# Optimization experiments

Measured on AMD Instinct MI355X. Metric: run time of the kernel, lower is better.

## Reference

```python
import jax, jax.numpy as jnp
import numpy as np

DN = ('NCHW', 'OIHW', 'NCHW')

def conv(x, w, b, stride=1, pad=0):
    y = jax.lax.conv_general_dilated(x, w, (stride, stride), ((pad, pad), (pad, pad)), dimension_numbers=DN)
    return y + b[None, :, None, None]

def maxpool(x, k, s):
    return jax.lax.reduce_window(x, -jnp.inf, jax.lax.max, (1, 1, k, k), (1, 1, s, s), 'VALID')

def bilinear_resize(x, oh, ow):
    # torch F.interpolate(mode='bilinear', align_corners=False)
    H, W = x.shape[2], x.shape[3]
    def grid(n_in, n_out):
        c = (jnp.arange(n_out, dtype=x.dtype) + 0.5) * (n_in / n_out) - 0.5
        c = jnp.clip(c, 0.0, n_in - 1)
        lo = jnp.floor(c).astype(jnp.int32)
        hi = jnp.minimum(lo + 1, n_in - 1)
        return lo, hi, c - lo
    r0, r1, wr = grid(H, oh)
    c0, c1, wc = grid(W, ow)
    top = x[:, :, r0, :] * (1 - wr)[None, None, :, None] + x[:, :, r1, :] * wr[None, None, :, None]
    return top[:, :, :, c0] * (1 - wc) + top[:, :, :, c1] * wc

def setup_inputs():
    key = jax.random.key(0)
    ks = jax.random.split(key, 18)
    s = 0.02
    d = {}
    d['x'] = jax.random.normal(ks[0], (16, 3, 448, 448), jnp.float32)
    d['w1'] = jax.random.normal(ks[1], (64, 3, 7, 7), jnp.float32) * s
    d['b1'] = jax.random.normal(ks[2], (64,), jnp.float32) * s
    d['w3'] = jax.random.normal(ks[3], (192, 64, 3, 3), jnp.float32) * s
    d['b3'] = jax.random.normal(ks[4], (192,), jnp.float32) * s
    d['w4'] = jax.random.normal(ks[5], (256, 192, 3, 3), jnp.float32) * s
    d['b4'] = jax.random.normal(ks[6], (256,), jnp.float32) * s
    d['w7'] = jax.random.normal(ks[7], (512, 256, 2, 2), jnp.float32) * s
    d['b7'] = jax.random.normal(ks[8], (512,), jnp.float32) * s
    d['w8'] = jax.random.normal(ks[9], (1024, 512, 2, 2), jnp.float32) * s
    d['b8'] = jax.random.normal(ks[10], (1024,), jnp.float32) * s
    d['wu'] = jax.random.normal(ks[11], (1024, 1024, 2, 2), jnp.float32) * s
    d['bu'] = jax.random.normal(ks[12], (1024,), jnp.float32) * s
    d['lc_w'] = jax.random.normal(ks[13], (1024, 256, 7, 7, 3, 3), jnp.float32) * s
    d['lc_b'] = jax.random.normal(ks[14], (256, 7, 7), jnp.float32) * s
    d['fc_w'] = jax.random.normal(ks[15], (4949, 12544), jnp.float32) * s  # S*S*(C+B*5)=7*7*101
    d['fc_b'] = jax.random.normal(ks[16], (4949,), jnp.float32) * s
    return d

def reference(x, w1, b1, w3, b3, w4, b4, w7, b7, w8, b8, wu, bu, lc_w, lc_b, fc_w, fc_b):
    x = conv(x, w1, b1, 2, 3)        # [B,64,224,224]
    x = maxpool(x, 2, 2)             # 112
    x = conv(x, w3, b3, 1, 1)        # [B,192,112,112]
    x = maxpool(x, 2, 2)             # 56
    x = conv(x, w4, b4)              # [B,256,54,54]
    x = maxpool(x, 2, 2)             # 27
    # CombinedNet backbone not defined in source listing: identity (256->256)
    x = conv(x, w7, b7)              # [B,512,26,26]
    x = maxpool(x, 2, 2)             # 13
    x = conv(x, w8, b8)              # [B,1024,12,12]
    x = conv(x, wu, bu)              # 11 (ultblock applied twice, shared weights)
    x = conv(x, wu, bu)              # 10
    x = maxpool(x, 5, 4)             # [B,1024,2,2]
    x = x[:, :, :14, :14]
    x = bilinear_resize(x, 7, 7)     # [B,1024,7,7]
    # LocallyConnected2d(1024,256,7,7,k=3,s=1,p=1) without materializing the unfold*weight product
    B = x.shape[0]
    xp = jnp.pad(x, ((0, 0), (0, 0), (1, 1), (1, 1)))
    patches = jnp.stack([xp[:, :, i:i + 7, j:j + 7] for i in range(3) for j in range(3)], axis=2)
    patches = patches.reshape(B, 1024, 3, 3, 7, 7)  # [B,C,kh,kw,H,W]
    y = jnp.einsum('bcijhw,cohwij->bohw', patches, lc_w) + lc_b[None]
    y = jnp.where(y > 0, y, 0.1 * y)  # LeakyReLU(0.1)
    # Dropout(p=0.5) is identity at inference; Linear
    y = y.reshape(B, -1) @ fc_w.T + fc_b  # [B,4949]
    return y.reshape(B, 7, 7, 101)
```

## Files before the change

### kernel.cpp

```cpp
#include <hip/hip_runtime.h>

#define UNR _Pragma("unroll")

typedef __attribute__((ext_vector_type(8))) short short8v;
typedef __attribute__((ext_vector_type(4))) float f32x4;

__device__ __forceinline__ ushort f2bf(float f) {
    union { float f; unsigned u; } x; x.f = f;
    unsigned r = (x.u + 0x7fffu + ((x.u >> 16) & 1u)) >> 16;
    return (ushort)r;
}
__device__ __forceinline__ float bf2f(ushort u) {
    union { unsigned u; float f; } x; x.u = ((unsigned)u) << 16;
    return x.f;
}

__device__ __forceinline__ void gll16(const ushort* gp, ushort* lp) {
    __builtin_amdgcn_global_load_lds(
        (const __attribute__((address_space(1))) unsigned int*)(const void*)gp,
        (__attribute__((address_space(3))) unsigned int*)(void*)lp, 16, 0, 0);
}

template<int Wp,int Hp,int OW,int OH,int WpN,int HpN,int PADN,int CN,int WAVES>
__global__ __launch_bounds__(WAVES*64)
void convc1(const ushort* __restrict__ Xp, const ushort* __restrict__ Wb,
            const float* __restrict__ bias, ushort* __restrict__ Yp)
{
    constexpr int CIN = 4, STRIDE = 2, NSTEP = 7;
    constexpr int POW = OW/2, POH = OH/2;
    constexpr int NTOT = 16*POW*POH*4;

    const int lane = (int)threadIdx.x & 63;
    const int wave = (int)threadIdx.x >> 6;
    const int n0   = (blockIdx.y*WAVES + wave) * 64;
    const int lm   = lane & 15;
    const int lk   = lane >> 4;

    int ns[4];
    unsigned boff[4];
    UNR for (int nf=0; nf<4; ++nf) {
        int n = n0 + nf*16 + lm;
        if (n > NTOT-1) n = NTOT-1;
        ns[nf] = n;
        int q = n & 3, pp = n >> 2;
        int px = pp % POW; int t = pp / POW;
        int py = t % POH;  int b = t / POH;
        int oy = 2*py + (q>>1), ox = 2*px + (q&1);
        boff[nf] = ((unsigned)(b*Hp + oy*STRIDE)*Wp + (unsigned)(ox*STRIDE))*CIN
                 + 8u*lk;
    }

    f32x4 acc[4][4];
    UNR for (int i=0;i<4;++i) UNR for (int j=0;j<4;++j) acc[i][j] = f32x4{0.f,0.f,0.f,0.f};

    auto ldfr = [&](int s, short8v (&a)[4], short8v (&bf)[4]) {
        const unsigned xoff = (unsigned)(s*Wp*CIN);
        UNR for (int mf=0; mf<4; ++mf)
            a[mf] = *(const short8v*)(Wb + (unsigned)((s*4 + mf)<<9) + (unsigned)lane*8);
        UNR for (int nf=0; nf<4; ++nf)
            bf[nf] = *(const short8v*)(Xp + boff[nf] + xoff);
    };
    auto dm = [&](short8v (&a)[4], short8v (&bf)[4]) {
        UNR for (int mf=0; mf<4; ++mf)
            UNR for (int nf=0; nf<4; ++nf)
                acc[mf][nf] = __builtin_amdgcn_mfma_f32_16x16x32_bf16(
                                  a[mf], bf[nf], acc[mf][nf], 0, 0, 0);
    };

    short8v aA[4], bA[4], aB[4], bB[4];
    ldfr(0, aA, bA);
    for (int sb = 0; sb < NSTEP; sb += 2) {
        if (sb+1 < NSTEP) ldfr(sb+1, aB, bB);
        dm(aA, bA);
        if (sb+2 < NSTEP) ldfr(sb+2, aA, bA);
        if (sb+1 < NSTEP) dm(aB, bB);
    }

    UNR for (int mf=0; mf<4; ++mf) {
        const int co = mf*16 + 4*lk;
        f32x4 bi = *(const f32x4*)(bias + co);
        UNR for (int nf=0; nf<4; ++nf) {
            f32x4 v = acc[mf][nf];
            UNR for (int r=0;r<4;++r) {
                float t2 = v[r] + bi[r];
                t2 = fmaxf(t2, __shfl_xor(t2 = t2, 1, 64));
                t2 = fmaxf(t2, __shfl_xor(t2, 2, 64));
                v[r] = t2;
            }
            if ((lane & 3) == 0 && (n0 + nf*16 + lm) < NTOT) {
                int pp = ns[nf] >> 2;
                int px = pp % POW; int t2 = pp / POW;
                int py = t2 % POH; int b = t2 / POH;
                unsigned off = ((unsigned)(b*HpN + py + PADN)*WpN
                                + (unsigned)(px + PADN))*CN + co;
                ushort4 s; s.x=f2bf(v[0]); s.y=f2bf(v[1]); s.z=f2bf(v[2]); s.w=f2bf(v[3]);
                *(ushort4*)(Yp + off) = s;
            }
        }
    }
}

template<int CIN,int K,int STRIDE,int Wp,int Hp,int OW,int OH,int COUT,
         bool POOL,int WpN,int HpN,int PADN,int CN,int MT,int NT,int SPLITS>
__global__ __launch_bounds__(256)
void convt(const ushort* __restrict__ Xp, const ushort* __restrict__ Wb,
           const float* __restrict__ bias, ushort* __restrict__ Yp,
           float* __restrict__ part)
{
    static_assert(MT*NT == 4, "4 waves");
    constexpr int POW = OW/2, POH = OH/2;
    constexpr int NTOT = POOL ? 16*POW*POH*4 : 16*OW*OH;
    constexpr int NCH = CIN/32, NSTEP = K*K*NCH;
    constexpr int SPS = NSTEP/SPLITS;
    constexpr int CA = MT*4, CPW = MT + NT;

    const int t    = (int)threadIdx.x;
    const int lane = t & 63;
    const int w    = t >> 6;
    const int mr   = w / NT, nc = w % NT;
    const int cy0  = blockIdx.x * MT;
    const int n0b  = blockIdx.y * (NT*64);
    const int nw0  = n0b + nc*64;
    const int lm   = lane & 15, lk = lane >> 4;
    const int s0   = blockIdx.z * SPS, sE = s0 + SPS;

    __shared__ __align__(1024) ushort Ab[2][CA*512];
    __shared__ __align__(1024) ushort Bb[2][NT*4*512];

    auto nmap = [&](int n, int& b, int& oy, int& ox) {
        if (n > NTOT-1) n = NTOT-1;
        if constexpr (POOL) {
            int q = n & 3, pp = n >> 2;
            int px = pp % POW; int tt = pp / POW;
            int py = tt % POH;  b = tt / POH;
            oy = 2*py + (q>>1); ox = 2*px + (q&1);
        } else {
            ox = n % OW; int tt = n / OW; oy = tt % OH; b = tt / OH;
        }
    };

    int ns[4];
    UNR for (int nf=0; nf<4; ++nf) {
        int n = nw0 + nf*16 + lm;
        if (n > NTOT-1) n = NTOT-1;
        ns[nf] = n;
    }

    unsigned bsrc[CPW];
    UNR for (int j=0; j<CPW; ++j) {
        int q = w*CPW + j;
        if (q >= CA) {
            int bq = q - CA;
            int n = n0b + bq*16 + (lane >> 2);
            int b, oy, ox; nmap(n, b, oy, ox);
            bsrc[j] = ((unsigned)(b*Hp + oy*STRIDE)*Wp + (unsigned)(ox*STRIDE))*CIN
                    + (unsigned)(lane & 3)*8u;
        } else bsrc[j] = 0;
    }

    auto xoffs = [&](int s) -> unsigned {
        int c0  = (s % NCH)*32;
        int kxy = s / NCH;
        int kx  = kxy % K, ky = kxy / K;
        return (unsigned)((ky*Wp + kx)*CIN + c0);
    };
    auto stage = [&](int s, int buf) {
        const unsigned xoff = xoffs(s);
        UNR for (int j=0; j<CPW; ++j) {
            int q = w*CPW + j;
            if (q < CA) {
                const ushort* src = Wb
                    + ((size_t)(((cy0 + (q>>2))*NSTEP + s)*4 + (q&3)) << 9)
                    + (unsigned)lane*8;
                gll16(src, &Ab[buf][(unsigned)q*512u + (unsigned)lane*8u]);
            } else {
                gll16(Xp + bsrc[j] + xoff,
                      &Bb[buf][(unsigned)(q-CA)*512u + (unsigned)lane*8u]);
            }
        }
    };

    f32x4 acc[4][4];
    UNR for (int i=0;i<4;++i) UNR for (int j=0;j<4;++j) acc[i][j] = f32x4{0.f,0.f,0.f,0.f};

    stage(s0, 0);
    __syncthreads();
    int buf = 0;
    for (int s = s0; s < sE; ++s) {
        if (s+1 < sE) stage(s+1, buf^1);
        short8v a[4], bf[4];
        UNR for (int mf=0; mf<4; ++mf)
            a[mf] = *(const short8v*)&Ab[buf][(unsigned)((mr*4+mf)*64 + lane)*8u];
        UNR for (int nf=0; nf<4; ++nf)
            bf[nf] = *(const short8v*)&Bb[buf][(unsigned)((nc*64 + nf*16 + lm)*4 + lk)*8u];
        UNR for (int mf=0; mf<4; ++mf)
            UNR for (int nf=0; nf<4; ++nf)
                acc[mf][nf] = __builtin_amdgcn_mfma_f32_16x16x32_bf16(
                                  a[mf], bf[nf], acc[mf][nf], 0, 0, 0);
        __syncthreads();
        buf ^= 1;
    }

    UNR for (int mf=0; mf<4; ++mf) {
        const int co = (cy0 + mr)*64 + mf*16 + 4*lk;
        if constexpr (SPLITS > 1) {
            UNR for (int nf=0; nf<4; ++nf) {
                if ((nw0 + nf*16 + lm) < NTOT)
                    *(f32x4*)(part + ((size_t)blockIdx.z*NTOT + ns[nf])*COUT + co)
                        = acc[mf][nf];
            }
        } else {
            f32x4 bi = *(const f32x4*)(bias + co);
            UNR for (int nf=0; nf<4; ++nf) {
                f32x4 v = acc[mf][nf];
                UNR for (int r=0;r<4;++r) v[r] += bi[r];
                if constexpr (POOL) {
                    UNR for (int r=0;r<4;++r) {
                        float tt = v[r];
                        tt = fmaxf(tt, __shfl_xor(tt, 1, 64));
                        tt = fmaxf(tt, __shfl_xor(tt, 2, 64));
                        v[r] = tt;
                    }
                    if ((lane & 3) == 0 && (nw0 + nf*16 + lm) < NTOT) {
                        int pp = ns[nf] >> 2;
                        int px = pp % POW; int t2 = pp / POW;
                        int py = t2 % POH; int b = t2 / POH;
                        unsigned off = ((unsigned)(b*HpN + py + PADN)*WpN
                                        + (unsigned)(px + PADN))*CN + co;
                        ushort4 s2; s2.x=f2bf(v[0]); s2.y=f2bf(v[1]); s2.z=f2bf(v[2]); s2.w=f2bf(v[3]);
                        *(ushort4*)(Yp + off) = s2;
                    }
                } else {
                    if ((nw0 + nf*16 + lm) < NTOT) {
                        int n = ns[nf];
                        int ox = n % OW; int t2 = n / OW; int oy = t2 % OH; int b = t2 / OH;
                        unsigned off = ((unsigned)(b*HpN + oy)*WpN + (unsigned)ox)*CN + co;
                        ushort4 s2; s2.x=f2bf(v[0]); s2.y=f2bf(v[1]); s2.z=f2bf(v[2]); s2.w=f2bf(v[3]);
                        *(ushort4*)(Yp + off) = s2;
                    }
                }
            }
        }
    }
}

template<int COUT,int OW,int OH,int WpN,int HpN,int CN,int SPLITS>
__global__ void kreduce(const float* __restrict__ part, const float* __restrict__ bias,
                        ushort* __restrict__ Yp) {
    constexpr int NTOT = 16*OW*OH;
    int idx = blockIdx.x*256 + (int)threadIdx.x;
    if (idx >= NTOT*COUT) return;
    int co = idx % COUT; int n = idx / COUT;
    float sum = 0.f;
    UNR for (int ks=0; ks<SPLITS; ++ks)
        sum += part[((size_t)ks*NTOT + n)*COUT + co];
    sum += bias[co];
    int ox = n % OW; int t = n / OW; int oy = t % OH; int b = t / OH;
    Yp[((unsigned)(b*HpN + oy)*WpN + (unsigned)ox)*CN + co] = f2bf(sum);
}

__global__ void x1build(const float* __restrict__ x, ushort* __restrict__ X1) {
    int idx = blockIdx.x*256 + (int)threadIdx.x;
    int xx = idx % 448; int t = idx/448; int y = t % 448; int b = t/448;
    const float* px = x + ((size_t)b*3*448 + y)*448 + xx;
    ushort4 s;
    s.x = f2bf(px[0]); s.y = f2bf(px[200704]); s.z = f2bf(px[401408]); s.w = 0;
    *(ushort4*)(X1 + ((unsigned)(b*456 + y+3)*456 + (unsigned)(xx+3))*4) = s;
}

__global__ void wcvt1(const float* __restrict__ w, ushort* __restrict__ o) {
    int idx = blockIdx.x*256 + (int)threadIdx.x;
    if (idx >= 14336) return;
    int e = idx & 7; int t = idx >> 3;
    int lane = t & 63; t >>= 6;
    int mf = t & 3; int s = t >> 2;
    int co = mf*16 + (lane & 15);
    int cc = (lane >> 4)*8 + e;
    int kx = cc >> 2, ci = cc & 3;
    float v = 0.f;
    if (kx < 7 && ci < 3) v = w[(((size_t)co*3 + ci)*7 + s)*7 + kx];
    o[idx] = f2bf(v);
}

template<int CIN,int K,int COUT>
__global__ void wcvt(const float* __restrict__ w, ushort* __restrict__ o) {
    constexpr int NCH = CIN/32, NSTEP = K*K*NCH;
    int idx = blockIdx.x*256 + (int)threadIdx.x;
    if (idx >= COUT*K*K*CIN) return;
    int e = idx & 7; int t = idx >> 3;
    int lane = t & 63; t >>= 6;
    int mf = t & 3; t >>= 2;
    int s = t % NSTEP; int cy = t / NSTEP;
    int co = cy*64 + mf*16 + (lane & 15);
    int kxy = s / NCH, ch = s % NCH;
    int ci = ch*32 + (lane >> 4)*8 + e;
    int ky = kxy / K, kx = kxy % K;
    o[idx] = f2bf(w[(((size_t)co*CIN + ci)*K + ky)*K + kx]);
}

__global__ void pool54_k(const ushort* __restrict__ in, float* __restrict__ out) {
    int idx = blockIdx.x*256 + (int)threadIdx.x;
    int c = idx & 1023; int t = idx >> 10; int q = t & 3; int b = t >> 2;
    int i = q >> 1, j = q & 1;
    float m = -1e30f;
    UNR for (int r=0;r<5;++r)
        UNR for (int cc=0;cc<5;++cc)
            m = fmaxf(m, bf2f(in[(((unsigned)(b*10 + i*4+r))*10 + (unsigned)(j*4+cc))*1024 + c]));
    out[((size_t)(b*1024 + c))*4 + q] = m;
}

__device__ __forceinline__ void bigrid(int k, int& lo, float& f) {
    float c = ((float)k + 0.5f) * (2.0f/7.0f) - 0.5f;
    c = fminf(fmaxf(c, 0.f), 1.f);
    float fl = floorf(c);
    lo = (int)fl;
    f = c - fl;
}

__global__ void buildPb(const float* __restrict__ pp, ushort* __restrict__ Pb) {
    int idx = blockIdx.x*256 + (int)threadIdx.x;
    int k = idx & 15;
    int c = (idx >> 4) & 1023;
    int r = idx >> 14;
    int b = r & 15; int hw = r >> 4;
    float val = 0.f;
    if (k < 9) {
        int i = k/3, j = k%3;
        int h = hw/7, w2 = hw%7;
        int rr = h + i - 1, cc = w2 + j - 1;
        if (rr>=0 && rr<7 && cc>=0 && cc<7) {
            int rlo; float rf; bigrid(rr, rlo, rf);
            int clo; float cf; bigrid(cc, clo, cf);
            int rhi = min(rlo+1,1), chi = min(clo+1,1);
            const float* qq = pp + ((size_t)(b*1024 + c))*4;
            float v00=qq[rlo*2+clo], v01=qq[rlo*2+chi], v10=qq[rhi*2+clo], v11=qq[rhi*2+chi];
            float top = v00*(1.f-cf) + v01*cf;
            float bot = v10*(1.f-cf) + v11*cf;
            val = top*(1.f-rf) + bot*rf;
        }
    }
    Pb[idx] = f2bf(val);
}

__global__ __launch_bounds__(256)
void lconv_fused(const float* __restrict__ lcw, const ushort* __restrict__ Pb,
                 float* __restrict__ part) {
    const int bid = (int)blockIdx.x;
    const int xcd = bid & 7;
    const int i   = bid >> 3;
    const int hw  = i % 49;
    const int ks  = xcd + 8*(i/49);
    const int t   = (int)threadIdx.x;
    const int lane = t & 63, w = t >> 6;
    const int lm = lane & 15, lk = lane >> 4;
    const int c0 = ks*64;

    __shared__ ushort A[2][8192];

    auto ldreg = [&](int cc, float (&w9)[2][9]) {
        const int cb = c0 + cc*2;
        UNR for (int cl=0; cl<2; ++cl) {
            const float* src = lcw + ((size_t)(cb+cl)*256 + (unsigned)(w*64+lane))*441
                             + hw*9;
            __builtin_memcpy(w9[cl], src, 36);
        }
    };
    auto wrlds = [&](int buf, float (&w9)[2][9]) {
        UNR for (int cl=0; cl<2; ++cl) {
            int rem = cl*256 + w*64 + lane;
            ushort u[16];
            UNR for (int k=0;k<8;++k) u[k]=f2bf(w9[cl][k]);
            u[8]=f2bf(w9[cl][8]);
            UNR for (int k=9;k<16;++k) u[k]=0;
            *(short8v*)&A[buf][(unsigned)rem*8u] = *(short8v*)&u[0];
            *(short8v*)&A[buf][4096u + (unsigned)rem*8u] = *(short8v*)&u[8];
        }
    };

    f32x4 acc[4];
    UNR for (int q=0;q<4;++q) acc[q] = f32x4{0.f,0.f,0.f,0.f};

    const ushort* Bb = Pb + (size_t)(hw*16 + lm)*16384 + ks*1024 + lk*8;
    const int arow = (lk&1)*512 + (lk>>1)*256 + w*64 + lm;

    auto mmac = [&](int buf, int cc) {
        short8v bv = *(const short8v*)(Bb + cc*32);
        UNR for (int mf = 0; mf < 4; ++mf) {
            short8v av = *(const short8v*)&A[buf][(unsigned)(arow + mf*16)*8u];
            acc[mf] = __builtin_amdgcn_mfma_f32_16x16x32_bf16(av, bv, acc[mf], 0,0,0);
        }
    };

    float wA[2][9], wB[2][9];
    ldreg(0, wA);
    wrlds(0, wA);
    ldreg(1, wB);
    for (int cc = 0; cc < 32; cc += 2) {
        mmac(0, cc);
        wrlds(1, wB);
        if (cc+2 < 32) ldreg(cc+2, wA);
        mmac(1, cc+1);
        if (cc+2 < 32) {
            wrlds(0, wA);
            if (cc+3 < 32) ldreg(cc+3, wB);
        }
    }

    UNR for (int mf=0; mf<4; ++mf)
        UNR for (int r=0;r<4;++r) {
            int o = w*64 + mf*16 + 4*lk + r;
            part[(((size_t)ks*49 + hw)*256 + o)*16 + lm] = acc[mf][r];
        }
}

__global__ void lreduce2(const float* __restrict__ part, const float* __restrict__ lcb,
                         float* __restrict__ yact) {
    int idx = blockIdx.x*256 + (int)threadIdx.x;
    int b = idx & 15; int o = (idx >> 4) & 255; int hw = idx >> 12;
    float sum = 0.f;
    UNR for (int ks=0; ks<16; ++ks)
        sum += part[(((size_t)ks*49 + hw)*256 + o)*16 + b];
    sum += lcb[o*49 + hw];
    float v = (sum > 0.f) ? sum : 0.1f*sum;
    yact[b*12544 + o*49 + hw] = v;
}

__global__ __launch_bounds__(256)
void fc_k(const float* __restrict__ act, const float* __restrict__ fw,
          const float* __restrict__ fb, float* __restrict__ out) {
    __shared__ float alds[16][256];
    __shared__ float red[4][4][16];
    const int t = (int)threadIdx.x;
    const int o0 = blockIdx.x*4;
    float acc[4][16];
    UNR for (int oo=0;oo<4;++oo) UNR for (int b=0;b<16;++b) acc[oo][b]=0.f;

    for (int k0=0; k0<12544; k0+=256) {
        __syncthreads();
        UNR for (int b=0;b<16;++b) alds[b][t] = act[b*12544 + k0 + t];
        __syncthreads();
        float wv[4];
        UNR for (int oo=0;oo<4;++oo) {
            int o = o0+oo;
            wv[oo] = (o < 4949) ? fw[(size_t)o*12544 + k0 + t] : 0.f;
        }
        UNR for (int b=0;b<16;++b) {
            float av = alds[b][t];
            UNR for (int oo=0;oo<4;++oo) acc[oo][b] = fmaf(wv[oo], av, acc[oo][b]);
        }
    }
    UNR for (int oo=0;oo<4;++oo)
        UNR for (int b=0;b<16;++b) {
            float v = acc[oo][b];
            UNR for (int off=32; off; off>>=1) v += __shfl_xor(v, off, 64);
            acc[oo][b] = v;
        }
    const int wave = t>>6, lane = t&63;
    if (lane == 0)
        UNR for (int oo=0;oo<4;++oo)
            UNR for (int b=0;b<16;++b) red[wave][oo][b] = acc[oo][b];
    __syncthreads();
    if (t < 64) {
        int oo = t>>4, b = t&15;
        float v = red[0][oo][b]+red[1][oo][b]+red[2][oo][b]+red[3][oo][b];
        int o = o0+oo;
        if (o < 4949) out[b*4949 + o] = v + fb[o];
    }
}

extern "C" void kernel_launch(void* const* d_in, const int* in_sizes, int n_in,
                              void* d_out, int out_size, void* d_ws, size_t ws_size,
                              hipStream_t stream) {
    const float* x   = (const float*)d_in[0];
    const float* w1  = (const float*)d_in[1];
    const float* b1  = (const float*)d_in[2];
    const float* w3  = (const float*)d_in[3];
    const float* b3  = (const float*)d_in[4];
    const float* w4  = (const float*)d_in[5];
    const float* b4  = (const float*)d_in[6];
    const float* w7  = (const float*)d_in[7];
    const float* b7  = (const float*)d_in[8];
    const float* w8  = (const float*)d_in[9];
    const float* b8  = (const float*)d_in[10];
    const float* wu  = (const float*)d_in[11];
    const float* bu  = (const float*)d_in[12];
    const float* lcw = (const float*)d_in[13];
    const float* lcb = (const float*)d_in[14];
    const float* fw  = (const float*)d_in[15];
    const float* fb  = (const float*)d_in[16];
    float* out = (float*)d_out;

    char* base = (char*)d_ws;
    auto alloc = [&](size_t bytes) { char* p = base; base += (bytes + 255) & ~(size_t)255; return p; };
    ushort* X1  = (ushort*)alloc(16u*456*456*4*2);
    ushort* X3  = (ushort*)alloc(16u*114*114*64*2);
    ushort* X4  = (ushort*)alloc(16u*56*56*192*2);
    ushort* X7  = (ushort*)alloc(16u*27*27*256*2);
    ushort* X8  = (ushort*)alloc(16u*13*13*512*2);
    ushort* XU1 = (ushort*)alloc(16u*12*12*1024*2);
    ushort* XU2 = (ushort*)alloc(16u*11*11*1024*2);
    ushort* XU3 = (ushort*)alloc(16u*10*10*1024*2);
    ushort* W1b = (ushort*)alloc(64u*224*2);
    ushort* W3b = (ushort*)alloc(192u*576*2);
    ushort* W4b = (ushort*)alloc(256u*1728*2);
    ushort* W7b = (ushort*)alloc(512u*1024*2);
    ushort* W8b = (ushort*)alloc(1024u*2048*2);
    ushort* WUb = (ushort*)alloc(1024u*4096*2);
    float*  pp  = (float*)alloc(16u*1024*4*4);
    ushort* Pb  = (ushort*)alloc((size_t)49*16*16384*2);
    float*  part = (float*)alloc((size_t)16*49*256*16*4);
    float*  partK = (float*)alloc((size_t)4*2304*1024*4);
    float*  yact = (float*)X7;

    hipMemsetAsync(X1, 0, 16u*456*456*4*2, stream);
    hipMemsetAsync(X3, 0, 16u*114*114*64*2, stream);
    x1build<<<12544, 256, 0, stream>>>(x, X1);
    wcvt1<<<56, 256, 0, stream>>>(w1, W1b);
    wcvt<64,3,192><<<432, 256, 0, stream>>>(w3, W3b);
    wcvt<192,3,256><<<1728, 256, 0, stream>>>(w4, W4b);
    wcvt<256,2,512><<<2048, 256, 0, stream>>>(w7, W7b);
    wcvt<512,2,1024><<<8192, 256, 0, stream>>>(w8, W8b);
    wcvt<1024,2,1024><<<16384, 256, 0, stream>>>(wu, WUb);

    convc1<456,456,224,224,114,114,1,64, 4>
        <<<dim3(1,3136), 256, 0, stream>>>(X1, W1b, b1, X3);
    convt<64,3,1,114,114,112,112,192, true,56,56,0,192, 1,4,1>
        <<<dim3(3,784,1), 256, 0, stream>>>(X3, W3b, b3, X4, nullptr);
    convt<192,3,1,56,56,54,54,256, true,27,27,0,256, 2,2,1>
        <<<dim3(2,365,1), 256, 0, stream>>>(X4, W4b, b4, X7, nullptr);
    convt<256,2,1,27,27,26,26,512, true,13,13,0,512, 2,2,1>
        <<<dim3(4,85,1), 256, 0, stream>>>(X7, W7b, b7, X8, nullptr);
    convt<512,2,1,13,13,12,12,1024, false,12,12,0,1024, 2,2,4>
        <<<dim3(8,18,4), 256, 0, stream>>>(X8, W8b, nullptr, nullptr, partK);
    kreduce<1024,12,12,12,12,1024,4><<<9216, 256, 0, stream>>>(partK, b8, XU1);
    convt<1024,2,1,12,12,11,11,1024, false,11,11,0,1024, 2,2,4>
        <<<dim3(8,16,4), 256, 0, stream>>>(XU1, WUb, nullptr, nullptr, partK);
    kreduce<1024,11,11,11,11,1024,4><<<7744, 256, 0, stream>>>(partK, bu, XU2);
    convt<1024,2,1,11,11,10,10,1024, false,10,10,0,1024, 2,2,4>
        <<<dim3(8,13,4), 256, 0, stream>>>(XU2, WUb, nullptr, nullptr, partK);
    kreduce<1024,10,10,10,10,1024,4><<<6400, 256, 0, stream>>>(partK, bu, XU3);

    pool54_k<<<256, 256, 0, stream>>>(XU3, pp);
    buildPb<<<50176, 256, 0, stream>>>(pp, Pb);
    lconv_fused<<<784, 256, 0, stream>>>(lcw, Pb, part);
    lreduce2<<<784, 256, 0, stream>>>(part, lcb, yact);
    fc_k<<<1238, 256, 0, stream>>>(yact, fw, fb, out);
}
```

Before: 806.7 us.

## Fuse padding into x1build, zero only X3 border, remap conv3 blocks, raise MFMA priority

The full-buffer memsets of X1 and X3 are replaced. x1build now writes every padded pixel, including zeros, and a new x3ring kernel zeroes only the one-pixel border of X3, which avoids rewriting the whole buffer. The 3x3 conv3 launch becomes a 1D grid remapped so that consecutive blocks spread across 8 chunks, likely aimed at XCD or L2 locality. The MFMA loop is wrapped in s_setprio to favour the matrix instructions. This assumes the interior of X3 is fully overwritten by convc1, which must hold for the result to stay correct.

After: 784.9 us. 2.7% less time.

```diff
diff --git a/kernel.cpp b/kernel.cpp
--- a/kernel.cpp
+++ b/kernel.cpp
@@ -83,7 +83,7 @@
             f32x4 v = acc[mf][nf];
             UNR for (int r=0;r<4;++r) {
                 float t2 = v[r] + bi[r];
-                t2 = fmaxf(t2, __shfl_xor(t2 = t2, 1, 64));
+                t2 = fmaxf(t2, __shfl_xor(t2, 1, 64));
                 t2 = fmaxf(t2, __shfl_xor(t2, 2, 64));
                 v[r] = t2;
             }
@@ -101,7 +101,8 @@
 }
 
 template<int CIN,int K,int STRIDE,int Wp,int Hp,int OW,int OH,int COUT,
-         bool POOL,int WpN,int HpN,int PADN,int CN,int MT,int NT,int SPLITS>
+         bool POOL,int WpN,int HpN,int PADN,int CN,int MT,int NT,int SPLITS,
+         int LINX=0,int LINY=0>
 __global__ __launch_bounds__(256)
 void convt(const ushort* __restrict__ Xp, const ushort* __restrict__ Wb,
            const float* __restrict__ bias, ushort* __restrict__ Yp,
@@ -112,20 +113,30 @@
     constexpr int NTOT = POOL ? 16*POW*POH*4 : 16*OW*OH;
     constexpr int NCH = CIN/32, NSTEP = K*K*NCH;
     constexpr int SPS = NSTEP/SPLITS;
-    constexpr int CA = MT*4, CPW = MT + NT;
+    constexpr int CA = MT*4, CB = NT*4, CPW = MT + NT;
+
+    int bx, by;
+    if constexpr (LINX > 0) {
+        constexpr int CHUNK = LINX*LINY/8;
+        int bid = (int)blockIdx.x;
+        int p = (bid & 7)*CHUNK + (bid >> 3);
+        bx = p % LINX; by = p / LINX;
+    } else {
+        bx = (int)blockIdx.x; by = (int)blockIdx.y;
+    }
 
     const int t    = (int)threadIdx.x;
     const int lane = t & 63;
     const int w    = t >> 6;
     const int mr   = w / NT, nc = w % NT;
-    const int cy0  = blockIdx.x * MT;
-    const int n0b  = blockIdx.y * (NT*64);
+    const int cy0  = bx * MT;
+    const int n0b  = by * (NT*64);
     const int nw0  = n0b + nc*64;
     const int lm   = lane & 15, lk = lane >> 4;
     const int s0   = blockIdx.z * SPS, sE = s0 + SPS;
 
     __shared__ __align__(1024) ushort Ab[2][CA*512];
-    __shared__ __align__(1024) ushort Bb[2][NT*4*512];
+    __shared__ __align__(1024) ushort Bb[2][CB*512];
 
     auto nmap = [&](int n, int& b, int& oy, int& ox) {
         if (n > NTOT-1) n = NTOT-1;
@@ -183,20 +194,26 @@
     f32x4 acc[4][4];
     UNR for (int i=0;i<4;++i) UNR for (int j=0;j<4;++j) acc[i][j] = f32x4{0.f,0.f,0.f,0.f};
 
+    auto compute = [&](int buf) {
+        short8v a[4], bf[4];
+        UNR for (int mf=0; mf<4; ++mf)
+            a[mf] = *(const short8v*)&Ab[buf][(unsigned)((mr*4+mf)*64 + lane)*8u];
+        UNR for (int nf=0; nf<4; ++nf)
+            bf[nf] = *(const short8v*)&Bb[buf][(unsigned)((nc*64 + nf*16 + lm)*4 + lk)*8u];
+        __builtin_amdgcn_s_setprio(1);
+        UNR for (int mf=0; mf<4; ++mf)
+            UNR for (int nf=0; nf<4; ++nf)
+                acc[mf][nf] = __builtin_amdgcn_mfma_f32_16x16x32_bf16(
+                                  a[mf], bf[nf], acc[mf][nf], 0, 0, 0);
+        __builtin_amdgcn_s_setprio(0);
+    };
+
     stage(s0, 0);
     __syncthreads();
     int buf = 0;
     for (int s = s0; s < sE; ++s) {
         if (s+1 < sE) stage(s+1, buf^1);
-        short8v a[4], bf[4];
-        UNR for (int mf=0; mf<4; ++mf)
-            a[mf] = *(const short8v*)&Ab[buf][(unsigned)((mr*4+mf)*64 + lane)*8u];
-        UNR for (int nf=0; nf<4; ++nf)
-            bf[nf] = *(const short8v*)&Bb[buf][(unsigned)((nc*64 + nf*16 + lm)*4 + lk)*8u];
-        UNR for (int mf=0; mf<4; ++mf)
-            UNR for (int nf=0; nf<4; ++nf)
-                acc[mf][nf] = __builtin_amdgcn_mfma_f32_16x16x32_bf16(
-                                  a[mf], bf[nf], acc[mf][nf], 0, 0, 0);
+        compute(buf);
         __syncthreads();
         buf ^= 1;
     }
@@ -261,11 +278,32 @@
 
 __global__ void x1build(const float* __restrict__ x, ushort* __restrict__ X1) {
     int idx = blockIdx.x*256 + (int)threadIdx.x;
-    int xx = idx % 448; int t = idx/448; int y = t % 448; int b = t/448;
-    const float* px = x + ((size_t)b*3*448 + y)*448 + xx;
-    ushort4 s;
-    s.x = f2bf(px[0]); s.y = f2bf(px[200704]); s.z = f2bf(px[401408]); s.w = 0;
-    *(ushort4*)(X1 + ((unsigned)(b*456 + y+3)*456 + (unsigned)(xx+3))*4) = s;
+    int xx = idx % 456; int t = idx/456; int y = t % 456; int b = t/456;
+    ushort4 s; s.x = 0; s.y = 0; s.z = 0; s.w = 0;
+    if (xx >= 3 && xx < 451 && y >= 3 && y < 451) {
+        const float* px = x + ((size_t)b*3*448 + (y-3))*448 + (xx-3);
+        s.x = f2bf(px[0]); s.y = f2bf(px[200704]); s.z = f2bf(px[401408]);
+    }
+    *(ushort4*)(X1 + ((unsigned)(b*456 + y)*456 + (unsigned)xx)*4) = s;
+}
+
+__global__ void x3ring(ushort* __restrict__ X3) {
+    int idx = blockIdx.x*256 + (int)threadIdx.x;
+    if (idx >= 462848) return;
+    int b = idx / 28928; int j = idx % 28928;
+    unsigned off;
+    if (j < 14592) {
+        int r = j / 7296; int rem = j % 7296;
+        int y = r ? 113 : 0;
+        off = ((unsigned)(b*114 + y)*114)*64u + (unsigned)rem;
+    } else {
+        int j2 = j - 14592;
+        int y = 1 + j2/128;
+        int rem = j2 % 128;
+        int xx = (rem >> 6) ? 113 : 0;
+        off = (((unsigned)(b*114 + y)*114) + (unsigned)xx)*64u + (unsigned)(rem & 63);
+    }
+    X3[off] = 0;
 }
 
 __global__ void wcvt1(const float* __restrict__ w, ushort* __restrict__ o) {
@@ -512,9 +550,8 @@
     float*  partK = (float*)alloc((size_t)4*2304*1024*4);
     float*  yact = (float*)X7;
 
-    hipMemsetAsync(X1, 0, 16u*456*456*4*2, stream);
-    hipMemsetAsync(X3, 0, 16u*114*114*64*2, stream);
-    x1build<<<12544, 256, 0, stream>>>(x, X1);
+    x1build<<<12996, 256, 0, stream>>>(x, X1);
+    x3ring<<<1808, 256, 0, stream>>>(X3);
     wcvt1<<<56, 256, 0, stream>>>(w1, W1b);
     wcvt<64,3,192><<<432, 256, 0, stream>>>(w3, W3b);
     wcvt<192,3,256><<<1728, 256, 0, stream>>>(w4, W4b);
@@ -524,8 +561,8 @@
 
     convc1<456,456,224,224,114,114,1,64, 4>
         <<<dim3(1,3136), 256, 0, stream>>>(X1, W1b, b1, X3);
-    convt<64,3,1,114,114,112,112,192, true,56,56,0,192, 1,4,1>
-        <<<dim3(3,784,1), 256, 0, stream>>>(X3, W3b, b3, X4, nullptr);
+    convt<64,3,1,114,114,112,112,192, true,56,56,0,192, 1,4,1, 3,784>
+        <<<2352, 256, 0, stream>>>(X3, W3b, b3, X4, nullptr);
     convt<192,3,1,56,56,54,54,256, true,27,27,0,256, 2,2,1>
         <<<dim3(2,365,1), 256, 0, stream>>>(X4, W4b, b4, X7, nullptr);
     convt<256,2,1,27,27,26,26,512, true,13,13,0,512, 2,2,1>
```
